# Kernel optimization log

Hardware: AMD Instinct MI355X
Metric: run time of the kernel (lower is better)

Reference implementation:

```python
import jax, jax.numpy as jnp
import numpy as np

MODEL_DIM = 1024
NUM_HEAD = 16
HEAD_DIM = MODEL_DIM // NUM_HEAD
B, S = 2, 2048


def setup_inputs() -> dict:
    key = jax.random.key(0)
    ks = jax.random.split(key, 13)
    s = 1.0 / np.sqrt(MODEL_DIM)
    inp = {
        "q": jax.random.normal(ks[0], (B, S, MODEL_DIM), jnp.float32),
        "k": jax.random.normal(ks[1], (B, S, MODEL_DIM), jnp.float32),
        "v": jax.random.normal(ks[2], (B, S, MODEL_DIM), jnp.float32),
        "mask": jax.random.randint(ks[3], (S, S), 0, 2, jnp.int32),
        "w_q": jax.random.normal(ks[4], (MODEL_DIM, MODEL_DIM), jnp.float32) * s,
        "b_q": jax.random.normal(ks[5], (MODEL_DIM,), jnp.float32) * s,
        "w_k": jax.random.normal(ks[6], (MODEL_DIM, MODEL_DIM), jnp.float32) * s,
        "b_k": jax.random.normal(ks[7], (MODEL_DIM,), jnp.float32) * s,
        "w_v": jax.random.normal(ks[8], (MODEL_DIM, MODEL_DIM), jnp.float32) * s,
        "b_v": jax.random.normal(ks[9], (MODEL_DIM,), jnp.float32) * s,
        "w_o": jax.random.normal(ks[10], (MODEL_DIM, MODEL_DIM), jnp.float32) * s,
        "b_o": jax.random.normal(ks[11], (MODEL_DIM,), jnp.float32) * s,
    }
    return inp


def reference(q, k, v, mask, w_q, b_q, w_k, b_k, w_v, b_v, w_o, b_o):
    batch, seq_len, dim = q.shape
    # Linear projections (weights stored as [d_in, d_out])
    Q = q @ w_q + b_q
    K = k @ w_k + b_k
    V = v @ w_v + b_v
    # [B, H, S, Dh]
    Q = Q.reshape(batch, seq_len, NUM_HEAD, HEAD_DIM).transpose(0, 2, 1, 3)
    K = K.reshape(batch, seq_len, NUM_HEAD, HEAD_DIM).transpose(0, 2, 1, 3)
    V = V.reshape(batch, seq_len, NUM_HEAD, HEAD_DIM).transpose(0, 2, 1, 3)
    scores = jnp.einsum("bhqd,bhkd->bhqk", Q, K) / jnp.sqrt(
        jnp.asarray(HEAD_DIM, Q.dtype)
    )
    scores = jnp.where(mask == 0, jnp.asarray(-1e9, scores.dtype), scores)
    attn = jax.nn.softmax(scores, axis=-1)
    out = jnp.einsum("bhqk,bhkd->bhqd", attn, V)
    out = out.transpose(0, 2, 1, 3).reshape(batch, seq_len, dim)
    return out @ w_o + b_o
```

## Files before the change

### kernel.cpp

```cpp
#include <hip/hip_runtime.h>
#include <stdint.h>

typedef __bf16 bf16;
typedef _Float16 f16;
typedef __attribute__((ext_vector_type(4))) __bf16 bf16x4;
typedef __attribute__((ext_vector_type(8))) __bf16 bf16x8;
typedef __attribute__((ext_vector_type(8))) _Float16 f16x8;
typedef __attribute__((ext_vector_type(4))) float f32x4;
typedef __attribute__((ext_vector_type(2))) float f32x2;

constexpr int S = 2048;
constexpr int D = 1024;
constexpr int H = 16;
constexpr int DH = 64;
constexpr int M = 4096;

constexpr float QSCALE = 0.18033688011112042f;

__device__ __forceinline__ void async16(void* lds, const void* g) {
  __builtin_amdgcn_global_load_lds(
      (const __attribute__((address_space(1))) void*)g,
      (__attribute__((address_space(3))) void*)lds, 16, 0, 0);
}

__global__ __launch_bounds__(256) void prep(
    const int* __restrict__ mask, uint64_t* __restrict__ MB,
    const float* __restrict__ q, const float* __restrict__ k,
    const float* __restrict__ v, bf16* __restrict__ qA, bf16* __restrict__ kA,
    bf16* __restrict__ vA, const float* __restrict__ Wq,
    const float* __restrict__ Wk, const float* __restrict__ Wv,
    const float* __restrict__ Wo, bf16* __restrict__ WTq,
    bf16* __restrict__ WTk, bf16* __restrict__ WTv, f16* __restrict__ WoT) {
  __shared__ float T[64 * 68];
  const int bid = blockIdx.x;
  const int tid = threadIdx.x;

  if (bid < 16384) {
    const int gid = bid * 4 + (tid >> 6);
    const int lane = tid & 63;
    const int kt = gid >> 11;
    const int qq = gid & (S - 1);
    int mv = mask[(size_t)qq * S + kt * 64 + lane];
    uint64_t bits = __ballot(mv != 0);
    if (lane == 0) MB[(size_t)kt * S + qq] = bits;
    return;
  }

  if (bid < 28672) {
    const int idx = bid - 16384;
    const int z = idx >> 12;
    const int x = idx & 4095;
    const float* src = (z == 0) ? q : (z == 1) ? k : v;
    bf16* dst = (z == 0) ? qA : (z == 1) ? kA : vA;
    const size_t i = ((size_t)x * 256 + tid) * 4;
    f32x4 xv = *(const f32x4*)(src + i);
    bf16x4 o;
#pragma unroll
    for (int j = 0; j < 4; j++) o[j] = (bf16)xv[j];
    *(bf16x4*)(dst + i) = o;
    return;
  }

  const int idx = bid - 28672;
  const int z = idx >> 8;
  const int xy = idx & 255;
  const int n0 = (xy >> 4) * 64, k0 = (xy & 15) * 64;
  const float* W = (z == 0) ? Wq : (z == 1) ? Wk : (z == 2) ? Wv : Wo;
  const int lr = tid >> 4, lc = (tid & 15) * 4;
#pragma unroll
  for (int r = 0; r < 4; r++) {
    f32x4 vv = *(const f32x4*)(W + (size_t)(k0 + r * 16 + lr) * 1024 + n0 + lc);
    *(f32x4*)&T[(r * 16 + lr) * 68 + lc] = vv;
  }
  __syncthreads();
  const int nn = tid >> 3, kc = (tid & 7) * 8;
#pragma unroll
  for (int p = 0; p < 2; p++) {
    int n = p * 32 + nn;
    if (z < 3) {
      bf16x8 h;
#pragma unroll
      for (int j = 0; j < 8; j++) h[j] = (bf16)T[(kc + j) * 68 + n];
      bf16* WT = (z == 0) ? WTq : (z == 1) ? WTk : WTv;
      *(bf16x8*)(WT + (size_t)(n0 + n) * 1024 + k0 + kc) = h;
    } else {
      f16x8 hf;
#pragma unroll
      for (int j = 0; j < 8; j++) hf[j] = (f16)T[(kc + j) * 68 + n];
      *(f16x8*)(WoT + (size_t)(n0 + n) * 1024 + k0 + kc) = hf;
    }
  }
}

__global__ __launch_bounds__(256) void gemm_qkv(
    const bf16* __restrict__ Aq, const bf16* __restrict__ Ak,
    const bf16* __restrict__ Av, const bf16* __restrict__ WTq,
    const bf16* __restrict__ WTk, const bf16* __restrict__ WTv,
    const float* __restrict__ bq, const float* __restrict__ bk,
    const float* __restrict__ bv, bf16* __restrict__ Qb,
    bf16* __restrict__ Kb, bf16* __restrict__ VT) {
  __shared__ char smem[34816];

  const int z = blockIdx.z;
  const bf16* A = (z == 0) ? Aq : (z == 1) ? Ak : Av;
  const bf16* WT = (z == 0) ? WTq : (z == 1) ? WTk : WTv;
  const float* bias = (z == 0) ? bq : (z == 1) ? bk : bv;
  const float oscale = (z == 0) ? QSCALE : 1.0f;

  const int tid = threadIdx.x;
  const int bn = blockIdx.x * 128;
  const int bm = blockIdx.y * 128;
  const int wv = tid >> 6;
  const int lane = tid & 63;
  const int quad = lane >> 4;
  const int lo = lane & 15;
  const int wm = (wv >> 1) * 64;
  const int wn = (wv & 1) * 64;

  f32x4 acc[4][4];
#pragma unroll
  for (int i = 0; i < 4; i++)
#pragma unroll
    for (int j = 0; j < 4; j++) acc[i][j] = {0.f, 0.f, 0.f, 0.f};

  const int rloc = lane >> 3;
  const int gx = (lane & 7) ^ rloc;
  const int rx = (lo & 7);

  for (int kt = 0; kt < 16; ++kt) {
#pragma unroll
    for (int j = 0; j < 4; j++) {
      int ch = wv * 4 + j;
      async16(smem + ch * 1024,
              A + (size_t)(bm + ch * 8 + rloc) * 1024 + kt * 64 + gx * 8);
      async16(smem + 16384 + ch * 1024,
              WT + (size_t)(bn + ch * 8 + rloc) * 1024 + kt * 64 + gx * 8);
    }
    __syncthreads();

#pragma unroll
    for (int ks = 0; ks < 2; ks++) {
      bf16x8 af[4], bfr[4];
#pragma unroll
      for (int mi = 0; mi < 4; mi++)
        af[mi] = *(const bf16x8*)(smem + (wm + mi * 16 + lo) * 128 +
                                  (((ks * 4 + quad) ^ rx) * 16));
#pragma unroll
      for (int ni = 0; ni < 4; ni++)
        bfr[ni] = *(const bf16x8*)(smem + 16384 + (wn + ni * 16 + lo) * 128 +
                                   (((ks * 4 + quad) ^ rx) * 16));
#pragma unroll
      for (int mi = 0; mi < 4; mi++)
#pragma unroll
        for (int ni = 0; ni < 4; ni++)
          acc[mi][ni] = __builtin_amdgcn_mfma_f32_16x16x32_bf16(
              af[mi], bfr[ni], acc[mi][ni], 0, 0, 0);
    }
    __syncthreads();
  }

  const int b = bm >> 11;
  const int srow0 = bm & (S - 1);

  if (z == 2) {
#pragma unroll
    for (int mi = 0; mi < 4; mi++)
#pragma unroll
      for (int ni = 0; ni < 4; ni++) {
        int col = bn + wn + ni * 16 + lo;
        int h = col >> 6, dh = col & 63;
        float bvv = bias[col];
        bf16x4 t;
#pragma unroll
        for (int r = 0; r < 4; r++) t[r] = (bf16)(acc[mi][ni][r] + bvv);
        int s0 = srow0 + wm + mi * 16 + quad * 4;
        *(bf16x4*)&VT[(((size_t)(b * H + h)) * DH + dh) * S + s0] = t;
      }
    return;
  }

  bf16* T = (bf16*)smem;
#pragma unroll
  for (int mi = 0; mi < 4; mi++)
#pragma unroll
    for (int ni = 0; ni < 4; ni++) {
      int col = wn + ni * 16 + lo;
      float bvv = bias[bn + col];
#pragma unroll
      for (int r = 0; r < 4; r++) {
        int row = wm + mi * 16 + quad * 4 + r;
        T[row * 136 + col] = (bf16)((acc[mi][ni][r] + bvv) * oscale);
      }
    }
  __syncthreads();
  bf16* out = (z == 0) ? Qb : Kb;
  const int rr = tid >> 1;
  const int half = tid & 1;
  const int h = (bn >> 6) + half;
  bf16* gp = out + (((size_t)(b * H + h)) * S + srow0 + rr) * DH;
#pragma unroll
  for (int j = 0; j < 8; j++)
    *(bf16x8*)(gp + j * 8) = *(const bf16x8*)&T[rr * 136 + half * 64 + j * 8];
}

__global__ __launch_bounds__(256) void gemm_o(
    const f16* __restrict__ A, const f16* __restrict__ WT,
    const float* __restrict__ bias, float* __restrict__ out) {
  __shared__ char smem[32768];

  const int tid = threadIdx.x;
  const int bn = blockIdx.x * 128;
  const int bm = blockIdx.y * 128;
  const int wv = tid >> 6;
  const int lane = tid & 63;
  const int quad = lane >> 4;
  const int lo = lane & 15;
  const int wm = (wv >> 1) * 64;
  const int wn = (wv & 1) * 64;

  f32x4 acc[4][4];
#pragma unroll
  for (int i = 0; i < 4; i++)
#pragma unroll
    for (int j = 0; j < 4; j++) acc[i][j] = {0.f, 0.f, 0.f, 0.f};

  const int rloc = lane >> 3;
  const int gx = (lane & 7) ^ rloc;
  const int rx = (lo & 7);

  for (int kt = 0; kt < 16; ++kt) {
#pragma unroll
    for (int j = 0; j < 4; j++) {
      int ch = wv * 4 + j;
      async16(smem + ch * 1024,
              A + (size_t)(bm + ch * 8 + rloc) * 1024 + kt * 64 + gx * 8);
      async16(smem + 16384 + ch * 1024,
              WT + (size_t)(bn + ch * 8 + rloc) * 1024 + kt * 64 + gx * 8);
    }
    __syncthreads();

#pragma unroll
    for (int ks = 0; ks < 2; ks++) {
      f16x8 af[4], bfr[4];
#pragma unroll
      for (int mi = 0; mi < 4; mi++)
        af[mi] = *(const f16x8*)(smem + (wm + mi * 16 + lo) * 128 +
                                 (((ks * 4 + quad) ^ rx) * 16));
#pragma unroll
      for (int ni = 0; ni < 4; ni++)
        bfr[ni] = *(const f16x8*)(smem + 16384 + (wn + ni * 16 + lo) * 128 +
                                  (((ks * 4 + quad) ^ rx) * 16));
#pragma unroll
      for (int mi = 0; mi < 4; mi++)
#pragma unroll
        for (int ni = 0; ni < 4; ni++)
          acc[mi][ni] = __builtin_amdgcn_mfma_f32_16x16x32_f16(
              af[mi], bfr[ni], acc[mi][ni], 0, 0, 0);
    }
    __syncthreads();
  }

#pragma unroll
  for (int mi = 0; mi < 4; mi++)
#pragma unroll
    for (int ni = 0; ni < 4; ni++) {
      int col = bn + wn + ni * 16 + lo;
      float bvv = bias[col];
#pragma unroll
      for (int r = 0; r < 4; r++) {
        int row = bm + wm + mi * 16 + quad * 4 + r;
        out[(size_t)row * 1024 + col] = acc[mi][ni][r] + bvv;
      }
    }
}

__global__ __launch_bounds__(512) void attn_kernel(
    const bf16* __restrict__ Qg, const bf16* __restrict__ Kg,
    const bf16* __restrict__ VTg, const uint64_t* __restrict__ MB,
    f16* __restrict__ AO) {
  __shared__ char smem[49152];

  const int tid = threadIdx.x;
  const int wv = tid >> 6;
  const int lane = tid & 63;
  const int quad = lane >> 4;
  const int lo = lane & 15;

  const int lin = blockIdx.x;
  const int bh = (lin & 7) * 4 + ((lin >> 3) & 3);
  const int qt = lin >> 5;
  const int qbase = qt * 128 + wv * 16;
  const size_t base = (size_t)bh * S * DH;
  bf16* Pw = (bf16*)(smem + 32768 + wv * 2048);
  const int xm = (lo & 7) << 1;

  const int c0 = wv * 2;
  const int rloc = lane >> 3;
  const int gx = (lane & 7) ^ rloc;
  const int rx = lo & 7;

  bf16x8 qf[2];
  {
    const bf16* qp = Qg + base + (size_t)(qbase + lo) * DH + quad * 8;
    qf[0] = *(const bf16x8*)qp;
    qf[1] = *(const bf16x8*)(qp + 32);
  }

  f32x4 Oacc[4];
#pragma unroll
  for (int j = 0; j < 4; j++) Oacc[j] = {0.f, 0.f, 0.f, 0.f};
  f32x2 lp = {0.f, 0.f};

#define STAGE(kt_, buf_)                                                       \
  {                                                                            \
    _Pragma("unroll") for (int j = 0; j < 2; j++) {                            \
      int c = c0 + j;                                                          \
      if (c < 8) {                                                             \
        async16((buf_) + c * 1024,                                             \
                Kg + base + (size_t)((kt_)*64 + c * 8 + rloc) * 64 + gx * 8);  \
      } else {                                                                 \
        int cv = c - 8;                                                        \
        async16((buf_) + 8192 + cv * 1024,                                     \
                VTg + base + (size_t)(cv * 8 + rloc) * S + (kt_)*64 + gx * 8); \
      }                                                                        \
    }                                                                          \
  }

  STAGE(0, smem);
  uint64_t mcur = MB[(size_t)0 * S + qbase + lo];

  for (int kt = 0; kt < 32; ++kt) {
    const char* cur = smem + (kt & 1) * 16384;

    uint64_t m0 = mcur >> (quad * 4);
    uint32_t mw[2] = {(uint32_t)m0, (uint32_t)(m0 >> 32)};

    __syncthreads();
    if (kt + 1 < 32) {
      STAGE(kt + 1, smem + ((kt + 1) & 1) * 16384);
      mcur = MB[(size_t)(kt + 1) * S + qbase + lo];
    }

    const char* Kls = cur;
    const char* Vls = cur + 8192;

    f32x4 sacc[4];
#pragma unroll
    for (int mi = 0; mi < 4; mi++) sacc[mi] = {0.f, 0.f, 0.f, 0.f};
    __builtin_amdgcn_s_setprio(1);
#pragma unroll
    for (int mi = 0; mi < 4; mi++) {
      bf16x8 k0 = *(const bf16x8*)(Kls + (mi * 16 + lo) * 128 + ((quad ^ rx) * 16));
      bf16x8 k1 = *(const bf16x8*)(Kls + (mi * 16 + lo) * 128 + (((4 + quad) ^ rx) * 16));
      sacc[mi] = __builtin_amdgcn_mfma_f32_16x16x32_bf16(k0, qf[0], sacc[mi], 0, 0, 0);
      sacc[mi] = __builtin_amdgcn_mfma_f32_16x16x32_bf16(k1, qf[1], sacc[mi], 0, 0, 0);
    }
    __builtin_amdgcn_s_setprio(0);

#pragma unroll
    for (int mi = 0; mi < 4; mi++) {
      bf16x4 t;
#pragma unroll
      for (int r = 0; r < 4; r++) {
        float p = __builtin_amdgcn_exp2f(sacc[mi][r]);
        int ext = __builtin_amdgcn_sbfe((int)mw[mi >> 1], ((mi & 1) << 4) + r, 1);
        p = __builtin_bit_cast(float, __builtin_bit_cast(int, p) & ext);
        lp[r & 1] += p;
        t[r] = (bf16)p;
      }
      *(bf16x4*)&Pw[lo * 64 + (((mi * 4 + quad) ^ xm) * 4)] = t;
    }

    __builtin_amdgcn_s_setprio(1);
#pragma unroll
    for (int kk = 0; kk < 2; kk++) {
      int g16 = kk * 8 + quad * 2;
      bf16x8 pa = *(const bf16x8*)&Pw[lo * 64 + ((g16 ^ xm) * 4)];
#pragma unroll
      for (int ni = 0; ni < 4; ni++) {
        bf16x8 vb = *(const bf16x8*)(Vls + (ni * 16 + lo) * 128 +
                                     (((kk * 4 + quad) ^ rx) * 16));
        Oacc[ni] = __builtin_amdgcn_mfma_f32_16x16x32_bf16(pa, vb, Oacc[ni], 0, 0, 0);
      }
    }
    __builtin_amdgcn_s_setprio(0);
  }
#undef STAGE

  float lpart = lp[0] + lp[1];
  lpart += __shfl_xor(lpart, 16);
  lpart += __shfl_xor(lpart, 32);

  const int b = bh >> 4, h = bh & (H - 1);
#pragma unroll
  for (int r = 0; r < 4; r++) {
    float inv = 1.0f / __shfl(lpart, quad * 4 + r);
    int q = qbase + quad * 4 + r;
    size_t rowoff = (size_t)(b * S + q) * D + h * DH;
#pragma unroll
    for (int ni = 0; ni < 4; ni++)
      AO[rowoff + ni * 16 + lo] = (f16)(Oacc[ni][r] * inv);
  }
}

extern "C" void kernel_launch(void* const* d_in, const int* in_sizes, int n_in,
                              void* d_out, int out_size, void* d_ws,
                              size_t ws_size, hipStream_t stream) {
  const float* q = (const float*)d_in[0];
  const float* k = (const float*)d_in[1];
  const float* v = (const float*)d_in[2];
  const int* mask = (const int*)d_in[3];
  const float* w_q = (const float*)d_in[4];
  const float* b_q = (const float*)d_in[5];
  const float* w_k = (const float*)d_in[6];
  const float* b_k = (const float*)d_in[7];
  const float* w_v = (const float*)d_in[8];
  const float* b_v = (const float*)d_in[9];
  const float* w_o = (const float*)d_in[10];
  const float* b_o = (const float*)d_in[11];

  char* w = (char*)d_ws;
  const size_t MiB = 1ull << 20;
  bf16* Qb = (bf16*)w;
  bf16* Kb = (bf16*)(w + 8 * MiB);
  bf16* VT = (bf16*)(w + 16 * MiB);
  bf16* qA = (bf16*)(w + 24 * MiB);
  bf16* kA = (bf16*)(w + 32 * MiB);
  bf16* vA = (bf16*)(w + 40 * MiB);
  f16* AO = (f16*)(w + 24 * MiB);
  bf16* WTq = (bf16*)(w + 48 * MiB);
  bf16* WTk = (bf16*)(w + 50 * MiB);
  bf16* WTv = (bf16*)(w + 52 * MiB);
  f16* WoT = (f16*)(w + 54 * MiB);
  uint64_t* MBits = (uint64_t*)(w + 58 * MiB);

  prep<<<29696, 256, 0, stream>>>(mask, MBits, q, k, v, qA, kA, vA, w_q, w_k,
                                  w_v, w_o, WTq, WTk, WTv, WoT);
  gemm_qkv<<<dim3(8, 32, 3), 256, 0, stream>>>(qA, kA, vA, WTq, WTk, WTv, b_q,
                                               b_k, b_v, Qb, Kb, VT);
  attn_kernel<<<dim3(512), 512, 0, stream>>>(Qb, Kb, VT, MBits, AO);
  gemm_o<<<dim3(8, 32), 256, 0, stream>>>(AO, WoT, b_o, (float*)d_out);
}
```

Measured before the change: 254.5 us.

## Store Q/K in row-major token layout and halve gemm_o M-tile

The QKV GEMM now writes Q and K directly in [B*S, 1024] row-major layout instead of restaging them through LDS into per-head [B,H,S,64] layout. The attention kernel reads Q and K with a row stride of 1024, removing an LDS round-trip and a barrier from the GEMM epilogue. The output-projection GEMM uses 64-row tiles, doubling its grid to 512 blocks to fill more compute units. The trade-off is scattered 2-byte stores in the QKV epilogue and strided K loads in attention, plus less operand reuse per gemm_o block.

```diff
diff --git a/kernel.cpp b/kernel.cpp
--- a/kernel.cpp
+++ b/kernel.cpp
@@ -99,7 +99,7 @@
     const float* __restrict__ bq, const float* __restrict__ bk,
     const float* __restrict__ bv, bf16* __restrict__ Qb,
     bf16* __restrict__ Kb, bf16* __restrict__ VT) {
-  __shared__ char smem[34816];
+  __shared__ char smem[32768];
 
   const int z = blockIdx.z;
   const bf16* A = (z == 0) ? Aq : (z == 1) ? Ak : Av;
@@ -159,10 +159,9 @@
     __syncthreads();
   }
 
-  const int b = bm >> 11;
-  const int srow0 = bm & (S - 1);
-
   if (z == 2) {
+    const int b = bm >> 11;
+    const int srow0 = bm & (S - 1);
 #pragma unroll
     for (int mi = 0; mi < 4; mi++)
 #pragma unroll
@@ -179,48 +178,39 @@
     return;
   }
 
-  bf16* T = (bf16*)smem;
+  bf16* out = (z == 0) ? Qb : Kb;
 #pragma unroll
   for (int mi = 0; mi < 4; mi++)
 #pragma unroll
     for (int ni = 0; ni < 4; ni++) {
-      int col = wn + ni * 16 + lo;
-      float bvv = bias[bn + col];
+      int col = bn + wn + ni * 16 + lo;
+      float bvv = bias[col];
 #pragma unroll
       for (int r = 0; r < 4; r++) {
-        int row = wm + mi * 16 + quad * 4 + r;
-        T[row * 136 + col] = (bf16)((acc[mi][ni][r] + bvv) * oscale);
+        int row = bm + wm + mi * 16 + quad * 4 + r;
+        out[(size_t)row * 1024 + col] = (bf16)((acc[mi][ni][r] + bvv) * oscale);
       }
     }
-  __syncthreads();
-  bf16* out = (z == 0) ? Qb : Kb;
-  const int rr = tid >> 1;
-  const int half = tid & 1;
-  const int h = (bn >> 6) + half;
-  bf16* gp = out + (((size_t)(b * H + h)) * S + srow0 + rr) * DH;
-#pragma unroll
-  for (int j = 0; j < 8; j++)
-    *(bf16x8*)(gp + j * 8) = *(const bf16x8*)&T[rr * 136 + half * 64 + j * 8];
 }
 
 __global__ __launch_bounds__(256) void gemm_o(
     const f16* __restrict__ A, const f16* __restrict__ WT,
     const float* __restrict__ bias, float* __restrict__ out) {
-  __shared__ char smem[32768];
+  __shared__ char smem[24576];
 
   const int tid = threadIdx.x;
   const int bn = blockIdx.x * 128;
-  const int bm = blockIdx.y * 128;
+  const int bm = blockIdx.y * 64;
   const int wv = tid >> 6;
   const int lane = tid & 63;
   const int quad = lane >> 4;
   const int lo = lane & 15;
-  const int wm = (wv >> 1) * 64;
+  const int wm = (wv >> 1) * 32;
   const int wn = (wv & 1) * 64;
 
-  f32x4 acc[4][4];
-#pragma unroll
-  for (int i = 0; i < 4; i++)
+  f32x4 acc[2][4];
+#pragma unroll
+  for (int i = 0; i < 2; i++)
 #pragma unroll
     for (int j = 0; j < 4; j++) acc[i][j] = {0.f, 0.f, 0.f, 0.f};
 
@@ -230,28 +220,32 @@
 
   for (int kt = 0; kt < 16; ++kt) {
 #pragma unroll
+    for (int j = 0; j < 2; j++) {
+      int ch = wv * 2 + j;
+      async16(smem + ch * 1024,
+              A + (size_t)(bm + ch * 8 + rloc) * 1024 + kt * 64 + gx * 8);
+    }
+#pragma unroll
     for (int j = 0; j < 4; j++) {
       int ch = wv * 4 + j;
-      async16(smem + ch * 1024,
-              A + (size_t)(bm + ch * 8 + rloc) * 1024 + kt * 64 + gx * 8);
-      async16(smem + 16384 + ch * 1024,
+      async16(smem + 8192 + ch * 1024,
               WT + (size_t)(bn + ch * 8 + rloc) * 1024 + kt * 64 + gx * 8);
     }
     __syncthreads();
 
 #pragma unroll
     for (int ks = 0; ks < 2; ks++) {
-      f16x8 af[4], bfr[4];
-#pragma unroll
-      for (int mi = 0; mi < 4; mi++)
+      f16x8 af[2], bfr[4];
+#pragma unroll
+      for (int mi = 0; mi < 2; mi++)
         af[mi] = *(const f16x8*)(smem + (wm + mi * 16 + lo) * 128 +
                                  (((ks * 4 + quad) ^ rx) * 16));
 #pragma unroll
       for (int ni = 0; ni < 4; ni++)
-        bfr[ni] = *(const f16x8*)(smem + 16384 + (wn + ni * 16 + lo) * 128 +
+        bfr[ni] = *(const f16x8*)(smem + 8192 + (wn + ni * 16 + lo) * 128 +
                                   (((ks * 4 + quad) ^ rx) * 16));
 #pragma unroll
-      for (int mi = 0; mi < 4; mi++)
+      for (int mi = 0; mi < 2; mi++)
 #pragma unroll
         for (int ni = 0; ni < 4; ni++)
           acc[mi][ni] = __builtin_amdgcn_mfma_f32_16x16x32_f16(
@@ -261,7 +255,7 @@
   }
 
 #pragma unroll
-  for (int mi = 0; mi < 4; mi++)
+  for (int mi = 0; mi < 2; mi++)
 #pragma unroll
     for (int ni = 0; ni < 4; ni++) {
       int col = bn + wn + ni * 16 + lo;
@@ -290,7 +284,9 @@
   const int bh = (lin & 7) * 4 + ((lin >> 3) & 3);
   const int qt = lin >> 5;
   const int qbase = qt * 128 + wv * 16;
-  const size_t base = (size_t)bh * S * DH;
+  const int b = bh >> 4, h = bh & (H - 1);
+  const size_t vbase = (size_t)bh * S * DH;
+  const int hcol = h * 64;
   bf16* Pw = (bf16*)(smem + 32768 + wv * 2048);
   const int xm = (lo & 7) << 1;
 
@@ -301,7 +297,8 @@
 
   bf16x8 qf[2];
   {
-    const bf16* qp = Qg + base + (size_t)(qbase + lo) * DH + quad * 8;
+    const bf16* qp =
+        Qg + (size_t)(b * S + qbase + lo) * 1024 + hcol + quad * 8;
     qf[0] = *(const bf16x8*)qp;
     qf[1] = *(const bf16x8*)(qp + 32);
   }
@@ -317,11 +314,12 @@
       int c = c0 + j;                                                          \
       if (c < 8) {                                                             \
         async16((buf_) + c * 1024,                                             \
-                Kg + base + (size_t)((kt_)*64 + c * 8 + rloc) * 64 + gx * 8);  \
+                Kg + (size_t)(b * S + (kt_)*64 + c * 8 + rloc) * 1024 + hcol + \
+                    gx * 8);                                                   \
       } else {                                                                 \
         int cv = c - 8;                                                        \
         async16((buf_) + 8192 + cv * 1024,                                     \
-                VTg + base + (size_t)(cv * 8 + rloc) * S + (kt_)*64 + gx * 8); \
+                VTg + vbase + (size_t)(cv * 8 + rloc) * S + (kt_)*64 + gx * 8); \
       }                                                                        \
     }                                                                          \
   }
@@ -391,7 +389,6 @@
   lpart += __shfl_xor(lpart, 16);
   lpart += __shfl_xor(lpart, 32);
 
-  const int b = bh >> 4, h = bh & (H - 1);
 #pragma unroll
   for (int r = 0; r < 4; r++) {
     float inv = 1.0f / __shfl(lpart, quad * 4 + r);
@@ -439,5 +436,5 @@
   gemm_qkv<<<dim3(8, 32, 3), 256, 0, stream>>>(qA, kA, vA, WTq, WTk, WTv, b_q,
                                                b_k, b_v, Qb, Kb, VT);
   attn_kernel<<<dim3(512), 512, 0, stream>>>(Qb, Kb, VT, MBits, AO);
-  gemm_o<<<dim3(8, 32), 256, 0, stream>>>(AO, WoT, b_o, (float*)d_out);
-}
+  gemm_o<<<dim3(8, 64), 256, 0, stream>>>(AO, WoT, b_o, (float*)d_out);
+}
```

Result: no change. 252.2 us (-0.9%).

## Double-buffer QKV GEMM loads and halve output GEMM row tile

Applied to the files above, without the earlier changes.

The QKV projection GEMM now uses two LDS buffers with a 32-wide K step, so the async global-to-LDS load for the next tile is issued before the MFMAs on the current tile. This removes one barrier per iteration and lets memory traffic overlap with compute, using a new swizzled layout. The output projection GEMM shrinks its M tile from 128 to 64 rows and launches twice as many blocks, giving more parallelism across the 256 CUs. The cost is less operand reuse per block and a reworked LDS addressing scheme that must still read the right data.

```diff
diff --git a/kernel.cpp b/kernel.cpp
--- a/kernel.cpp
+++ b/kernel.cpp
@@ -114,53 +114,64 @@
   const int lane = tid & 63;
   const int quad = lane >> 4;
   const int lo = lane & 15;
+  const int wm4 = (wv >> 1) * 4096;
+  const int wn4 = (wv & 1) * 4096;
+
+  f32x4 acc[4][4];
+#pragma unroll
+  for (int i = 0; i < 4; i++)
+#pragma unroll
+    for (int j = 0; j < 4; j++) acc[i][j] = {0.f, 0.f, 0.f, 0.f};
+
+  const int pl = lane >> 3;
+  const int uu = lane & 7;
+  const int srow = pl * 2 + (uu & 1);
+  const int sg = (uu >> 1) ^ (pl & 3);
+  const int uread = (((quad ^ ((lo >> 1) & 3)) << 1) | (lo & 1)) * 16;
+  const int aoff = (lo >> 1) * 128 + uread;
+
+#define QSTAGE(kt_, buf_)                                                      \
+  {                                                                            \
+    _Pragma("unroll") for (int j = 0; j < 4; j++) {                            \
+      int c = wv * 4 + j;               \
+      if (c < 8) {                                                             \
+        async16((buf_) + c * 1024,                                             \
+                A + (size_t)(bm + c * 16 + srow) * 1024 + (kt_)*32 + sg * 8);  \
+      } else {                                                                 \
+        int cb = c - 8;                                                        \
+        async16((buf_) + 8192 + cb * 1024,                                     \
+                WT + (size_t)(bn + cb * 16 + srow) * 1024 + (kt_)*32 + sg * 8);\
+      }                                                                        \
+    }                                                                          \
+  }
+
+  QSTAGE(0, smem);
+
+  for (int kt = 0; kt < 32; ++kt) {
+    const char* cur = smem + (kt & 1) * 16384;
+    __syncthreads();
+    if (kt + 1 < 32) QSTAGE(kt + 1, smem + ((kt + 1) & 1) * 16384);
+
+    bf16x8 af[4], bfr[4];
+#pragma unroll
+    for (int mi = 0; mi < 4; mi++)
+      af[mi] = *(const bf16x8*)(cur + wm4 + mi * 1024 + aoff);
+#pragma unroll
+    for (int ni = 0; ni < 4; ni++)
+      bfr[ni] = *(const bf16x8*)(cur + 8192 + wn4 + ni * 1024 + aoff);
+#pragma unroll
+    for (int mi = 0; mi < 4; mi++)
+#pragma unroll
+      for (int ni = 0; ni < 4; ni++)
+        acc[mi][ni] = __builtin_amdgcn_mfma_f32_16x16x32_bf16(
+            af[mi], bfr[ni], acc[mi][ni], 0, 0, 0);
+  }
+#undef QSTAGE
+
+  const int b = bm >> 11;
+  const int srow0 = bm & (S - 1);
   const int wm = (wv >> 1) * 64;
   const int wn = (wv & 1) * 64;
-
-  f32x4 acc[4][4];
-#pragma unroll
-  for (int i = 0; i < 4; i++)
-#pragma unroll
-    for (int j = 0; j < 4; j++) acc[i][j] = {0.f, 0.f, 0.f, 0.f};
-
-  const int rloc = lane >> 3;
-  const int gx = (lane & 7) ^ rloc;
-  const int rx = (lo & 7);
-
-  for (int kt = 0; kt < 16; ++kt) {
-#pragma unroll
-    for (int j = 0; j < 4; j++) {
-      int ch = wv * 4 + j;
-      async16(smem + ch * 1024,
-              A + (size_t)(bm + ch * 8 + rloc) * 1024 + kt * 64 + gx * 8);
-      async16(smem + 16384 + ch * 1024,
-              WT + (size_t)(bn + ch * 8 + rloc) * 1024 + kt * 64 + gx * 8);
-    }
-    __syncthreads();
-
-#pragma unroll
-    for (int ks = 0; ks < 2; ks++) {
-      bf16x8 af[4], bfr[4];
-#pragma unroll
-      for (int mi = 0; mi < 4; mi++)
-        af[mi] = *(const bf16x8*)(smem + (wm + mi * 16 + lo) * 128 +
-                                  (((ks * 4 + quad) ^ rx) * 16));
-#pragma unroll
-      for (int ni = 0; ni < 4; ni++)
-        bfr[ni] = *(const bf16x8*)(smem + 16384 + (wn + ni * 16 + lo) * 128 +
-                                   (((ks * 4 + quad) ^ rx) * 16));
-#pragma unroll
-      for (int mi = 0; mi < 4; mi++)
-#pragma unroll
-        for (int ni = 0; ni < 4; ni++)
-          acc[mi][ni] = __builtin_amdgcn_mfma_f32_16x16x32_bf16(
-              af[mi], bfr[ni], acc[mi][ni], 0, 0, 0);
-    }
-    __syncthreads();
-  }
-
-  const int b = bm >> 11;
-  const int srow0 = bm & (S - 1);
 
   if (z == 2) {
 #pragma unroll
@@ -179,6 +190,7 @@
     return;
   }
 
+  __syncthreads();
   bf16* T = (bf16*)smem;
 #pragma unroll
   for (int mi = 0; mi < 4; mi++)
@@ -206,21 +218,21 @@
 __global__ __launch_bounds__(256) void gemm_o(
     const f16* __restrict__ A, const f16* __restrict__ WT,
     const float* __restrict__ bias, float* __restrict__ out) {
-  __shared__ char smem[32768];
+  __shared__ char smem[24576];
 
   const int tid = threadIdx.x;
   const int bn = blockIdx.x * 128;
-  const int bm = blockIdx.y * 128;
+  const int bm = blockIdx.y * 64;
   const int wv = tid >> 6;
   const int lane = tid & 63;
   const int quad = lane >> 4;
   const int lo = lane & 15;
-  const int wm = (wv >> 1) * 64;
+  const int wm = (wv >> 1) * 32;
   const int wn = (wv & 1) * 64;
 
-  f32x4 acc[4][4];
-#pragma unroll
-  for (int i = 0; i < 4; i++)
+  f32x4 acc[2][4];
+#pragma unroll
+  for (int i = 0; i < 2; i++)
 #pragma unroll
     for (int j = 0; j < 4; j++) acc[i][j] = {0.f, 0.f, 0.f, 0.f};
 
@@ -230,28 +242,32 @@
 
   for (int kt = 0; kt < 16; ++kt) {
 #pragma unroll
+    for (int j = 0; j < 2; j++) {
+      int ch = wv * 2 + j;
+      async16(smem + ch * 1024,
+              A + (size_t)(bm + ch * 8 + rloc) * 1024 + kt * 64 + gx * 8);
+    }
+#pragma unroll
     for (int j = 0; j < 4; j++) {
       int ch = wv * 4 + j;
-      async16(smem + ch * 1024,
-              A + (size_t)(bm + ch * 8 + rloc) * 1024 + kt * 64 + gx * 8);
-      async16(smem + 16384 + ch * 1024,
+      async16(smem + 8192 + ch * 1024,
               WT + (size_t)(bn + ch * 8 + rloc) * 1024 + kt * 64 + gx * 8);
     }
     __syncthreads();
 
 #pragma unroll
     for (int ks = 0; ks < 2; ks++) {
-      f16x8 af[4], bfr[4];
-#pragma unroll
-      for (int mi = 0; mi < 4; mi++)
+      f16x8 af[2], bfr[4];
+#pragma unroll
+      for (int mi = 0; mi < 2; mi++)
         af[mi] = *(const f16x8*)(smem + (wm + mi * 16 + lo) * 128 +
                                  (((ks * 4 + quad) ^ rx) * 16));
 #pragma unroll
       for (int ni = 0; ni < 4; ni++)
-        bfr[ni] = *(const f16x8*)(smem + 16384 + (wn + ni * 16 + lo) * 128 +
+        bfr[ni] = *(const f16x8*)(smem + 8192 + (wn + ni * 16 + lo) * 128 +
                                   (((ks * 4 + quad) ^ rx) * 16));
 #pragma unroll
-      for (int mi = 0; mi < 4; mi++)
+      for (int mi = 0; mi < 2; mi++)
 #pragma unroll
         for (int ni = 0; ni < 4; ni++)
           acc[mi][ni] = __builtin_amdgcn_mfma_f32_16x16x32_f16(
@@ -261,7 +277,7 @@
   }
 
 #pragma unroll
-  for (int mi = 0; mi < 4; mi++)
+  for (int mi = 0; mi < 2; mi++)
 #pragma unroll
     for (int ni = 0; ni < 4; ni++) {
       int col = bn + wn + ni * 16 + lo;
@@ -439,5 +455,5 @@
   gemm_qkv<<<dim3(8, 32, 3), 256, 0, stream>>>(qA, kA, vA, WTq, WTk, WTv, b_q,
                                                b_k, b_v, Qb, Kb, VT);
   attn_kernel<<<dim3(512), 512, 0, stream>>>(Qb, Kb, VT, MBits, AO);
-  gemm_o<<<dim3(8, 32), 256, 0, stream>>>(AO, WoT, b_o, (float*)d_out);
-}
+  gemm_o<<<dim3(8, 64), 256, 0, stream>>>(AO, WoT, b_o, (float*)d_out);
+}
```

New measurement: 248.1 us. -2.5%, faster.
